# Optimization experiments

Hardware: AMD Instinct MI355X
Metric: run time of the kernel (lower is better)

## Reference

```python
import jax, jax.numpy as jnp
import numpy as np


def setup_inputs() -> dict:
    key = jax.random.key(0)
    k1, k2, k3, k4, k5 = jax.random.split(key, 5)
    B, N, M, K, D, O = 4, 32768, 8192, 16, 64, 64
    x = jax.random.normal(k1, (B, N, D), jnp.float32)
    x_subset = jax.random.normal(k2, (B, M, D), jnp.float32)
    knn_index = jax.random.randint(k3, (B, M, K), 0, N, jnp.int32)
    # 1x1 Conv2d(2*D -> O) == per-point linear: weight (O, 2D), bias (O,)
    W = jax.random.normal(k4, (O, 2 * D), jnp.float32) * (1.0 / np.sqrt(2 * D))
    b = jax.random.normal(k5, (O,), jnp.float32) * 0.01
    return {"x": x, "x_subset": x_subset, "knn_index": knn_index, "W": W, "b": b}


def reference(x, x_subset, knn_index, W, b):
    # knn_gather: (B,N,D) indexed by (B,M,K) -> (B,M,K,D)
    grouped = jax.vmap(lambda xb, ib: xb[ib])(x, knn_index)
    center = x_subset[:, :, None, :]                      # (B,M,1,D)
    edge = jnp.concatenate(
        [grouped - center, jnp.broadcast_to(center, grouped.shape)], axis=-1
    )                                                     # (B,M,K,2D)
    # 1x1 conv over channel dim + ReLU, output layout (B,O,M,K)
    h = jax.nn.relu(jnp.einsum("bmkc,oc->bomk", edge, W) + b[None, :, None, None])
    return jnp.max(h, axis=-1)                            # (B,O,M)
```

## Files before the change

kernel.cpp:

```cpp
#include <hip/hip_runtime.h>
#include <math.h>

#define B_ 4
#define N_ 32768
#define M_ 8192
#define K_ 16
#define D_ 64
#define O_ 64

typedef __attribute__((ext_vector_type(8))) short bf16x8;
typedef __attribute__((ext_vector_type(4))) float f32x4;

static __device__ __forceinline__ short f2bf(float f) {
    unsigned u = __float_as_uint(f);
    u += 0x7fffu + ((u >> 16) & 1u);
    return (short)(u >> 16);
}

static __device__ __forceinline__ bf16x8 cvt_bf8(float4 f0, float4 f1) {
    bf16x8 v;
    v[0] = f2bf(f0.x); v[1] = f2bf(f0.y); v[2] = f2bf(f0.z); v[3] = f2bf(f0.w);
    v[4] = f2bf(f1.x); v[5] = f2bf(f1.y); v[6] = f2bf(f1.z); v[7] = f2bf(f1.w);
    return v;
}

static __device__ __forceinline__ bf16x8 ld_bf8(const float* p) {
    return cvt_bf8(*(const float4*)p, *(const float4*)(p + 4));
}

#define PIN4(q) asm volatile("" :: "v"((q).x), "v"((q).y), "v"((q).z), "v"((q).w))

__global__ __launch_bounds__(512, 4)
void fused_gconv(const float* __restrict__ x, const float* __restrict__ xs,
                 const int* __restrict__ idx, const float* __restrict__ W,
                 const float* __restrict__ bias, float* __restrict__ out) {
    __shared__ int    ldsI[512];
    __shared__ bf16x8 ldsW[4][2][2][64];
    __shared__ float  ldsB[64];
    __shared__ float  ldsT[64 * 33];

    const int tid  = threadIdx.x;
    const int blk  = blockIdx.x;
    const int xcd  = blk & 7;
    const int slot = blk >> 3;
    const int bb   = xcd >> 1;
    const int m0   = (((xcd & 1) << 7) + slot) << 5;

    ldsI[tid] = idx[((size_t)bb * M_ + m0) * 16 + tid];

    const int l  = tid & 63;
    const int wv = tid >> 6;
    const int lr = l & 15;
    const int kg = l >> 4;

    {
        const int t = wv >> 1, s = wv & 1;
        const float* wp = W + (size_t)(t * 16 + lr) * 128 + s * 32 + kg * 8;
        float4 f0 = *(const float4*)wp;
        float4 f1 = *(const float4*)(wp + 4);
        float4 g0 = *(const float4*)(wp + 64);
        float4 g1 = *(const float4*)(wp + 68);
        ldsW[t][s][0][l] = cvt_bf8(f0, f1);
        float4 d0 = make_float4(g0.x - f0.x, g0.y - f0.y, g0.z - f0.z, g0.w - f0.w);
        float4 d1 = make_float4(g1.x - f1.x, g1.y - f1.y, g1.z - f1.z, g1.w - f1.w);
        ldsW[t][s][1][l] = cvt_bf8(d0, d1);
        if (tid < 64) ldsB[tid] = bias[tid];
    }
    __syncthreads();

    float binit[4];
    #pragma unroll
    for (int t = 0; t < 4; ++t) binit[t] = ldsB[t * 16 + lr];

    const float* xsp = xs + ((size_t)bb * M_ + m0 + (wv >> 2) * 16 + lr) * 64 + kg * 8;
    bf16x8 axs0 = ld_bf8(xsp);
    bf16x8 axs1 = ld_bf8(xsp + 32);

    float vout[4][4];
    #pragma unroll
    for (int t = 0; t < 4; ++t) {
        bf16x8 bd0 = ldsW[t][0][1][l];
        bf16x8 bd1 = ldsW[t][1][1][l];
        f32x4 a = {binit[t], binit[t], binit[t], binit[t]};
        a = __builtin_amdgcn_mfma_f32_16x16x32_bf16(axs0, bd0, a, 0, 0, 0);
        a = __builtin_amdgcn_mfma_f32_16x16x32_bf16(axs1, bd1, a, 0, 0, 0);
        vout[t][0] = a[0]; vout[t][1] = a[1];
        vout[t][2] = a[2]; vout[t][3] = a[3];
    }

    int rr[4];
    #pragma unroll
    for (int j = 0; j < 4; ++j)
        rr[j] = ldsI[(wv * 4 + j) * 16 + lr];

    const float* xb = x + (size_t)bb * N_ * 64;

    float4 q0[4], q1[4], q2[4], q3[4];
    #pragma unroll
    for (int j = 0; j < 4; ++j) {
        const float* xp = xb + (size_t)(unsigned)rr[j] * 64 + kg * 8;
        q0[j] = *(const float4*)xp;
        q1[j] = *(const float4*)(xp + 4);
        q2[j] = *(const float4*)(xp + 32);
        q3[j] = *(const float4*)(xp + 36);
    }
    #pragma unroll
    for (int j = 0; j < 4; ++j) {
        PIN4(q0[j]); PIN4(q1[j]); PIN4(q2[j]); PIN4(q3[j]);
    }

    bf16x8 a0[4], a1[4];
    #pragma unroll
    for (int j = 0; j < 4; ++j) {
        a0[j] = cvt_bf8(q0[j], q1[j]);
        a1[j] = cvt_bf8(q2[j], q3[j]);
    }

    float pv[4][4];
    #pragma unroll
    for (int t = 0; t < 4; ++t) {
        bf16x8 w0 = ldsW[t][0][0][l];
        bf16x8 w1 = ldsW[t][1][0][l];
        #pragma unroll
        for (int j = 0; j < 4; ++j) {
            f32x4 a = {0.f, 0.f, 0.f, 0.f};
            a = __builtin_amdgcn_mfma_f32_16x16x32_bf16(a0[j], w0, a, 0, 0, 0);
            a = __builtin_amdgcn_mfma_f32_16x16x32_bf16(a1[j], w1, a, 0, 0, 0);
            pv[t][j] = fmaxf(fmaxf(a[0], a[1]), fmaxf(a[2], a[3]));
        }
    }

    #pragma unroll
    for (int t = 0; t < 4; ++t)
        #pragma unroll
        for (int j = 0; j < 4; ++j) {
            float v = pv[t][j];
            v = fmaxf(v, __shfl_xor(v, 16));
            v = fmaxf(v, __shfl_xor(v, 32));
            if (kg == (wv & 3))
                vout[t][j] += v;
        }

    if (kg == (wv & 3)) {
        #pragma unroll
        for (int t = 0; t < 4; ++t)
            #pragma unroll
            for (int r = 0; r < 4; ++r) {
                float v = vout[t][r];
                ldsT[(t * 16 + lr) * 33 + wv * 4 + r] = v > 0.f ? v : 0.f;
            }
    }
    __syncthreads();

    const int o  = tid >> 3;
    const int ms = (tid & 7) * 4;
    const float* lp = &ldsT[o * 33 + ms];
    float4 v = make_float4(lp[0], lp[1], lp[2], lp[3]);
    *(float4*)(out + ((size_t)bb * 64 + o) * M_ + m0 + ms) = v;
}

extern "C" void kernel_launch(void* const* d_in, const int* in_sizes, int n_in,
                              void* d_out, int out_size, void* d_ws, size_t ws_size,
                              hipStream_t stream) {
    const float* x    = (const float*)d_in[0];
    const float* xs   = (const float*)d_in[1];
    const int*   idx  = (const int*)d_in[2];
    const float* W    = (const float*)d_in[3];
    const float* bias = (const float*)d_in[4];
    float* out = (float*)d_out;

    fused_gconv<<<(B_ * M_) / 32, 512, 0, stream>>>(x, xs, idx, W, bias, out);
}
```

Before: 30.70 us.

## Pre-convert x to bf16 in workspace so the gather reads half the bytes

Adds a streaming pre-pass kernel that converts all of x to bf16 in the workspace buffer. The fused kernel then gathers neighbor rows as bf16 directly, and those gather loads are issued earlier, before the center-point MFMA work. This halves the bytes moved by the random gather and removes the in-kernel conversion. In exchange it adds a full read of x, a half-size write, and a second kernel launch. A naive fallback kernel is used when the workspace is too small.

```diff
diff --git a/kernel.cpp b/kernel.cpp
--- a/kernel.cpp
+++ b/kernel.cpp
@@ -28,10 +28,27 @@
     return cvt_bf8(*(const float4*)p, *(const float4*)(p + 4));
 }
 
-#define PIN4(q) asm volatile("" :: "v"((q).x), "v"((q).y), "v"((q).z), "v"((q).w))
+#define PIN4I(q) asm volatile("" :: "v"((q).x), "v"((q).y), "v"((q).z), "v"((q).w))
+
+__global__ __launch_bounds__(256)
+void cvt_x(const float* __restrict__ x, short* __restrict__ xb) {
+    const int blk  = blockIdx.x;
+    const int xcd  = blk & 7;
+    const int slot = blk >> 3;
+    const int bb   = xcd >> 1;
+    const int half = xcd & 1;
+    const size_t base = (size_t)bb * N_ * 64 + ((size_t)(half * 256 + slot)) * 4096;
+    #pragma unroll
+    for (int i = 0; i < 2; ++i) {
+        size_t off = base + ((size_t)threadIdx.x + i * 256) * 8;
+        float4 f0 = *(const float4*)(x + off);
+        float4 f1 = *(const float4*)(x + off + 4);
+        *(bf16x8*)(xb + off) = cvt_bf8(f0, f1);
+    }
+}
 
 __global__ __launch_bounds__(512, 4)
-void fused_gconv(const float* __restrict__ x, const float* __restrict__ xs,
+void fused_gconv(const short* __restrict__ xb, const float* __restrict__ xs,
                  const int* __restrict__ idx, const float* __restrict__ W,
                  const float* __restrict__ bias, float* __restrict__ out) {
     __shared__ int    ldsI[512];
@@ -68,6 +85,22 @@
     }
     __syncthreads();
 
+    int rr[4];
+    #pragma unroll
+    for (int j = 0; j < 4; ++j)
+        rr[j] = ldsI[(wv * 4 + j) * 16 + lr];
+
+    const short* xbb = xb + (size_t)bb * N_ * 64;
+    int4 g0[4], g1[4];
+    #pragma unroll
+    for (int j = 0; j < 4; ++j) {
+        const short* xp = xbb + (size_t)(unsigned)rr[j] * 64 + kg * 8;
+        g0[j] = *(const int4*)xp;
+        g1[j] = *(const int4*)(xp + 32);
+    }
+    #pragma unroll
+    for (int j = 0; j < 4; ++j) { PIN4I(g0[j]); PIN4I(g1[j]); }
+
     float binit[4];
     #pragma unroll
     for (int t = 0; t < 4; ++t) binit[t] = ldsB[t * 16 + lr];
@@ -88,34 +121,6 @@
         vout[t][2] = a[2]; vout[t][3] = a[3];
     }
 
-    int rr[4];
-    #pragma unroll
-    for (int j = 0; j < 4; ++j)
-        rr[j] = ldsI[(wv * 4 + j) * 16 + lr];
-
-    const float* xb = x + (size_t)bb * N_ * 64;
-
-    float4 q0[4], q1[4], q2[4], q3[4];
-    #pragma unroll
-    for (int j = 0; j < 4; ++j) {
-        const float* xp = xb + (size_t)(unsigned)rr[j] * 64 + kg * 8;
-        q0[j] = *(const float4*)xp;
-        q1[j] = *(const float4*)(xp + 4);
-        q2[j] = *(const float4*)(xp + 32);
-        q3[j] = *(const float4*)(xp + 36);
-    }
-    #pragma unroll
-    for (int j = 0; j < 4; ++j) {
-        PIN4(q0[j]); PIN4(q1[j]); PIN4(q2[j]); PIN4(q3[j]);
-    }
-
-    bf16x8 a0[4], a1[4];
-    #pragma unroll
-    for (int j = 0; j < 4; ++j) {
-        a0[j] = cvt_bf8(q0[j], q1[j]);
-        a1[j] = cvt_bf8(q2[j], q3[j]);
-    }
-
     float pv[4][4];
     #pragma unroll
     for (int t = 0; t < 4; ++t) {
@@ -123,9 +128,11 @@
         bf16x8 w1 = ldsW[t][1][0][l];
         #pragma unroll
         for (int j = 0; j < 4; ++j) {
+            bf16x8 a0 = *(bf16x8*)&g0[j];
+            bf16x8 a1 = *(bf16x8*)&g1[j];
             f32x4 a = {0.f, 0.f, 0.f, 0.f};
-            a = __builtin_amdgcn_mfma_f32_16x16x32_bf16(a0[j], w0, a, 0, 0, 0);
-            a = __builtin_amdgcn_mfma_f32_16x16x32_bf16(a1[j], w1, a, 0, 0, 0);
+            a = __builtin_amdgcn_mfma_f32_16x16x32_bf16(a0, w0, a, 0, 0, 0);
+            a = __builtin_amdgcn_mfma_f32_16x16x32_bf16(a1, w1, a, 0, 0, 0);
             pv[t][j] = fmaxf(fmaxf(a[0], a[1]), fmaxf(a[2], a[3]));
         }
     }
@@ -159,6 +166,30 @@
     *(float4*)(out + ((size_t)bb * 64 + o) * M_ + m0 + ms) = v;
 }
 
+__global__ void naive_all(const float* __restrict__ x, const float* __restrict__ xs,
+                          const int* __restrict__ idx, const float* __restrict__ W,
+                          const float* __restrict__ bias, float* __restrict__ out) {
+    size_t t = (size_t)blockIdx.x * 256 + threadIdx.x;
+    if (t >= (size_t)B_ * O_ * M_) return;
+    int m = (int)(t % M_);
+    int o = (int)((t / M_) % O_);
+    int b = (int)(t / ((size_t)M_ * O_));
+    const float* xp = x + (size_t)b * N_ * D_;
+    const float* c  = xs + ((size_t)b * M_ + m) * D_;
+    const int*   id = idx + ((size_t)b * M_ + m) * K_;
+    const float* w1 = W + o * 128;
+    const float* w2 = w1 + 64;
+    float best = -INFINITY;
+    for (int k = 0; k < K_; ++k) {
+        const float* g = xp + (size_t)id[k] * D_;
+        float s = bias[o];
+        for (int d = 0; d < D_; ++d)
+            s += (g[d] - c[d]) * w1[d] + c[d] * w2[d];
+        best = fmaxf(best, s);
+    }
+    out[t] = best > 0.0f ? best : 0.0f;
+}
+
 extern "C" void kernel_launch(void* const* d_in, const int* in_sizes, int n_in,
                               void* d_out, int out_size, void* d_ws, size_t ws_size,
                               hipStream_t stream) {
@@ -169,5 +200,15 @@
     const float* bias = (const float*)d_in[4];
     float* out = (float*)d_out;
 
-    fused_gconv<<<(B_ * M_) / 32, 512, 0, stream>>>(x, xs, idx, W, bias, out);
-}
+    const size_t needXB = (size_t)B_ * N_ * 64 * sizeof(short);
+    if (ws_size < needXB) {
+        size_t total = (size_t)B_ * O_ * M_;
+        naive_all<<<(int)((total + 255) / 256), 256, 0, stream>>>(x, xs, idx, W, bias, out);
+        return;
+    }
+
+    short* xb = (short*)d_ws;
+
+    cvt_x<<<2048, 256, 0, stream>>>(x, xb);
+    fused_gconv<<<(B_ * M_) / 32, 512, 0, stream>>>(xb, xs, idx, W, bias, out);
+}
```

New measurement: 33.79 us. +10.1%, slower.
